# Performance work log

Hardware: AMD Instinct MI355X
Metric: run time of the kernel (lower is better)

The kernel has to match this reference:

```python
import jax, jax.numpy as jnp
import numpy as np

VOCAB = 32000
HID = 128
NUM_LAYERS = 2
B, T = 4, 2048


def setup_inputs() -> dict:
    key = jax.random.key(0)
    ks = jax.random.split(key, 12)
    s = 1.0 / np.sqrt(HID)
    inp = {
        "x": jax.random.randint(ks[0], (B, T), 0, VOCAB, dtype=jnp.int64),
        "hidden": jnp.zeros((NUM_LAYERS, B, HID), jnp.float32),
        "emb": jax.random.normal(ks[1], (VOCAB, HID), jnp.float32),
        "W_ih0": jax.random.uniform(ks[2], (HID, HID), jnp.float32, -s, s),
        "W_hh0": jax.random.uniform(ks[3], (HID, HID), jnp.float32, -s, s),
        "b_ih0": jax.random.uniform(ks[4], (HID,), jnp.float32, -s, s),
        "b_hh0": jax.random.uniform(ks[5], (HID,), jnp.float32, -s, s),
        "W_ih1": jax.random.uniform(ks[6], (HID, HID), jnp.float32, -s, s),
        "W_hh1": jax.random.uniform(ks[7], (HID, HID), jnp.float32, -s, s),
        "b_ih1": jax.random.uniform(ks[8], (HID,), jnp.float32, -s, s),
        "b_hh1": jax.random.uniform(ks[9], (HID,), jnp.float32, -s, s),
        "fc_w": jax.random.uniform(ks[10], (VOCAB, HID), jnp.float32, -s, s),
        "fc_b": jax.random.uniform(ks[11], (VOCAB,), jnp.float32, -s, s),
    }
    return inp


def _rnn_layer(x_seq, h0, W_ih, W_hh, b_ih, b_hh):
    # x_seq: [B, T, H]; h0: [B, H]. Elman RNN with tanh, like nn.RNN.
    def step(h, x_t):
        h_new = jnp.tanh(x_t @ W_ih.T + b_ih + h @ W_hh.T + b_hh)
        return h_new, h_new
    h_last, ys = jax.lax.scan(step, h0, jnp.swapaxes(x_seq, 0, 1))  # scan over T
    return jnp.swapaxes(ys, 0, 1), h_last  # [B,T,H], [B,H]


def reference(x, hidden, emb, W_ih0, W_hh0, b_ih0, b_hh0,
              W_ih1, W_hh1, b_ih1, b_hh1, fc_w, fc_b):
    out = emb[x]  # [B, T, H] embedding lookup
    out, h0 = _rnn_layer(out, hidden[0], W_ih0, W_hh0, b_ih0, b_hh0)
    out, h1 = _rnn_layer(out, hidden[1], W_ih1, W_hh1, b_ih1, b_hh1)
    logits = out @ fc_w.T + fc_b  # [B, T, VOCAB]
    new_hidden = jnp.stack([h0, h1], axis=0)  # [num_layers, B, H]
    return logits, new_hidden
```

## Files before the change

kernel.cpp:

```cpp
#include <hip/hip_runtime.h>

#define BB 4
#define TT 2048
#define HH 128
#define VV 32000

typedef __attribute__((ext_vector_type(8))) _Float16 half8;
typedef __attribute__((ext_vector_type(4))) float floatx4;

__global__ void preact_kernel(const float* __restrict__ src,
                              const int* __restrict__ idx,
                              const float* __restrict__ Wih,
                              const float* __restrict__ b1,
                              const float* __restrict__ b2,
                              float* __restrict__ out) {
    __shared__ float xs[HH];
    int row = blockIdx.x;
    int j = threadIdx.x;
    const float* srow = idx ? (src + (long)idx[row] * HH) : (src + (long)row * HH);
    xs[j] = srow[j];
    __syncthreads();
    const float* wrow = Wih + j * HH;
    float a0 = 0.f, a1 = 0.f, a2 = 0.f, a3 = 0.f;
#pragma unroll
    for (int k = 0; k < HH; k += 4) {
        float4 w = *(const float4*)(wrow + k);
        a0 += w.x * xs[k + 0];
        a1 += w.y * xs[k + 1];
        a2 += w.z * xs[k + 2];
        a3 += w.w * xs[k + 3];
    }
    out[(long)row * HH + j] = (a0 + a1) + (a2 + a3) + b1[j] + b2[j];
}

__global__ void __launch_bounds__(256, 1) rnn_fused_kernel(
        const float* __restrict__ pre0,
        const float* __restrict__ Whh0,
        const float* __restrict__ Wih1,
        const float* __restrict__ Whh1,
        const float* __restrict__ bih1,
        const float* __restrict__ bhh1,
        const float* __restrict__ hin,
        float* __restrict__ out1,
        float* __restrict__ hout) {
    __shared__ float hs0[2][HH];
    __shared__ float hs1[2][HH];
    const int b = blockIdx.x;
    const int tid = threadIdx.x;
    const int l = tid & 63;
    const int half = l >> 5;
    const int j = (tid >> 6) * 32 + (l & 31);

    float w0r[64];
    {
        const float* s = Whh0 + j * HH + half * 64;
#pragma unroll
        for (int q = 0; q < 16; q++) {
            float4 v = *(const float4*)(s + q * 4);
            w0r[4 * q + 0] = v.x; w0r[4 * q + 1] = v.y;
            w0r[4 * q + 2] = v.z; w0r[4 * q + 3] = v.w;
        }
    }
    float w1r[128];
    {
        const float* s = (half ? Whh1 : Wih1) + j * HH;
#pragma unroll
        for (int q = 0; q < 32; q++) {
            float4 v = *(const float4*)(s + q * 4);
            w1r[4 * q + 0] = v.x; w1r[4 * q + 1] = v.y;
            w1r[4 * q + 2] = v.z; w1r[4 * q + 3] = v.w;
        }
    }
    const float bias1 = bih1[j] + bhh1[j];

    if (tid < HH) {
        hs0[1][tid] = hin[b * HH + tid];
        hs1[0][tid] = hin[(BB + b) * HH + tid];
    }
    __syncthreads();

    const float* prow = pre0 + ((long)b * TT) * HH + j;
    float pnext = prow[0];
    for (int i = 0; i <= TT; i++) {
        const int rb = (i & 1) ^ 1;
        const int wb = i & 1;
        float p = pnext;
        if (i + 1 < TT) pnext = prow[(long)(i + 1) * HH];

        float a0 = 0.f, a1 = 0.f, a2 = 0.f, a3 = 0.f;
        if (i < TT) {
#pragma unroll
            for (int q = 0; q < 16; q++) {
                float4 h4 = *(const float4*)(&hs0[rb][half * 64 + q * 4]);
                a0 += h4.x * w0r[4 * q + 0];
                a1 += h4.y * w0r[4 * q + 1];
                a2 += h4.z * w0r[4 * q + 2];
                a3 += h4.w * w0r[4 * q + 3];
            }
        }
        float c0 = 0.f, c1 = 0.f, c2 = 0.f, c3 = 0.f;
        if (i >= 1) {
            const float* hsrc = half ? &hs1[rb][0] : &hs0[rb][0];
#pragma unroll
            for (int q = 0; q < 32; q++) {
                float4 h4 = *(const float4*)(hsrc + q * 4);
                c0 += h4.x * w1r[4 * q + 0];
                c1 += h4.y * w1r[4 * q + 1];
                c2 += h4.z * w1r[4 * q + 2];
                c3 += h4.w * w1r[4 * q + 3];
            }
        }
        float acc0 = (a0 + a1) + (a2 + a3);
        float acc1 = (c0 + c1) + (c2 + c3);
        acc0 += __shfl_xor(acc0, 32);
        acc1 += __shfl_xor(acc1, 32);
        float hnew = tanhf(half ? (acc1 + bias1) : (acc0 + p));
        if (half == 0) {
            if (i < TT) hs0[wb][j] = hnew;
        } else {
            if (i >= 1) {
                hs1[wb][j] = hnew;
                out1[((long)b * TT + (i - 1)) * HH + j] = hnew;
            }
        }
        __syncthreads();
    }
    if (tid < HH) {
        hout[b * HH + tid] = hs0[(TT - 1) & 1][tid];
        hout[(BB + b) * HH + tid] = hs1[TT & 1][tid];
    }
}

#define BM 64
#define BN 128
#define LDK 136

__global__ void __launch_bounds__(256) logits_kernel(
        const float* __restrict__ act,
        const float* __restrict__ fcw,
        const float* __restrict__ fcb,
        float* __restrict__ Cout) {
    __shared__ __align__(16) _Float16 As[BM * LDK];
    __shared__ __align__(16) _Float16 Bs[BN * LDK];
    const int bn = blockIdx.x;
    const int bm = blockIdx.y;
    const int tid = threadIdx.x;

#pragma unroll
    for (int s = 0; s < 8; s++) {
        int f = tid + s * 256;
        int r = f >> 5, c4 = f & 31;
        float4 v = *(const float4*)(act + ((long)(bm * BM + r)) * HH + c4 * 4);
        _Float16* d = &As[r * LDK + c4 * 4];
        d[0] = (_Float16)v.x; d[1] = (_Float16)v.y;
        d[2] = (_Float16)v.z; d[3] = (_Float16)v.w;
    }
#pragma unroll
    for (int s = 0; s < 16; s++) {
        int f = tid + s * 256;
        int r = f >> 5, c4 = f & 31;
        float4 v = *(const float4*)(fcw + ((long)(bn * BN + r)) * HH + c4 * 4);
        _Float16* d = &Bs[r * LDK + c4 * 4];
        d[0] = (_Float16)v.x; d[1] = (_Float16)v.y;
        d[2] = (_Float16)v.z; d[3] = (_Float16)v.w;
    }
    __syncthreads();

    const int wv = tid >> 6;
    const int wm = wv >> 1, wn = wv & 1;
    const int r = tid & 15, q = (tid & 63) >> 4;

    floatx4 acc[2][4];
#pragma unroll
    for (int mt = 0; mt < 2; mt++)
#pragma unroll
        for (int nt = 0; nt < 4; nt++) acc[mt][nt] = (floatx4){0.f, 0.f, 0.f, 0.f};

#pragma unroll
    for (int kk = 0; kk < 4; kk++) {
        half8 af[2], bf[4];
#pragma unroll
        for (int mt = 0; mt < 2; mt++)
            af[mt] = *(const half8*)(&As[(wm * 32 + mt * 16 + r) * LDK + kk * 32 + q * 8]);
#pragma unroll
        for (int nt = 0; nt < 4; nt++)
            bf[nt] = *(const half8*)(&Bs[(wn * 64 + nt * 16 + r) * LDK + kk * 32 + q * 8]);
#pragma unroll
        for (int mt = 0; mt < 2; mt++)
#pragma unroll
            for (int nt = 0; nt < 4; nt++)
                acc[mt][nt] = __builtin_amdgcn_mfma_f32_16x16x32_f16(af[mt], bf[nt], acc[mt][nt], 0, 0, 0);
    }

#pragma unroll
    for (int mt = 0; mt < 2; mt++) {
#pragma unroll
        for (int nt = 0; nt < 4; nt++) {
            int gcol = bn * BN + wn * 64 + nt * 16 + r;
            float bias = fcb[gcol];
#pragma unroll
            for (int r4 = 0; r4 < 4; r4++) {
                int grow = bm * BM + wm * 32 + mt * 16 + q * 4 + r4;
                Cout[(long)grow * VV + gcol] = acc[mt][nt][r4] + bias;
            }
        }
    }
}

extern "C" void kernel_launch(void* const* d_in, const int* in_sizes, int n_in,
                              void* d_out, int out_size, void* d_ws, size_t ws_size,
                              hipStream_t stream) {
    const int*   x      = (const int*)d_in[0];
    const float* hidden = (const float*)d_in[1];
    const float* emb    = (const float*)d_in[2];
    const float* Wih0   = (const float*)d_in[3];
    const float* Whh0   = (const float*)d_in[4];
    const float* bih0   = (const float*)d_in[5];
    const float* bhh0   = (const float*)d_in[6];
    const float* Wih1   = (const float*)d_in[7];
    const float* Whh1   = (const float*)d_in[8];
    const float* bih1   = (const float*)d_in[9];
    const float* bhh1   = (const float*)d_in[10];
    const float* fcw    = (const float*)d_in[11];
    const float* fcb    = (const float*)d_in[12];

    float* logits = (float*)d_out;
    float* hout   = logits + (long)BB * TT * VV;

    float* wsA = (float*)d_ws;
    float* ws1 = wsA + (long)BB * TT * HH;

    preact_kernel<<<BB * TT, HH, 0, stream>>>(emb, x, Wih0, bih0, bhh0, wsA);
    rnn_fused_kernel<<<BB, 256, 0, stream>>>(wsA, Whh0, Wih1, Whh1, bih1, bhh1,
                                             hidden, ws1, hout);
    logits_kernel<<<dim3(VV / BN, (BB * TT) / BM), 256, 0, stream>>>(ws1, fcw, fcb, logits);
}
```

Baseline: 3.717 ms.

## Split RNN layers across separate waves in a 512-thread block

The fused two-layer recurrence now runs with 512 threads. Waves 0-3 compute layer 1 and waves 4-7 compute layer 0, so each thread holds only one layer's weights and does one dot product per step instead of two. The cross-half reduction uses permlane32_swap instead of a shuffle, and __syncthreads is replaced by an explicit lgkmcnt wait plus s_barrier. This shortens each serial step's dependency chain but puts twice as many waves through every per-step barrier.

```diff
diff --git a/kernel.cpp b/kernel.cpp
--- a/kernel.cpp
+++ b/kernel.cpp
@@ -33,7 +33,7 @@
     out[(long)row * HH + j] = (a0 + a1) + (a2 + a3) + b1[j] + b2[j];
 }
 
-__global__ void __launch_bounds__(256, 1) rnn_fused_kernel(
+__global__ void __launch_bounds__(512, 1) rnn_fused_kernel(
         const float* __restrict__ pre0,
         const float* __restrict__ Whh0,
         const float* __restrict__ Wih1,
@@ -47,31 +47,31 @@
     __shared__ float hs1[2][HH];
     const int b = blockIdx.x;
     const int tid = threadIdx.x;
+    const int w = tid >> 6;
     const int l = tid & 63;
-    const int half = l >> 5;
-    const int j = (tid >> 6) * 32 + (l & 31);
-
-    float w0r[64];
-    {
-        const float* s = Whh0 + j * HH + half * 64;
+    const int part = l >> 5;
+    const bool isL1 = (w < 4);
+    const int j = (isL1 ? w : (w - 4)) * 32 + (l & 31);
+
+    float wreg[128];
+    if (isL1) {
+        const float* s = (part ? Whh1 : Wih1) + j * HH;
+#pragma unroll
+        for (int q = 0; q < 32; q++) {
+            float4 v = *(const float4*)(s + 4 * q);
+            wreg[4 * q + 0] = v.x; wreg[4 * q + 1] = v.y;
+            wreg[4 * q + 2] = v.z; wreg[4 * q + 3] = v.w;
+        }
+    } else {
+        const float* s = Whh0 + j * HH + part * 64;
 #pragma unroll
         for (int q = 0; q < 16; q++) {
-            float4 v = *(const float4*)(s + q * 4);
-            w0r[4 * q + 0] = v.x; w0r[4 * q + 1] = v.y;
-            w0r[4 * q + 2] = v.z; w0r[4 * q + 3] = v.w;
-        }
-    }
-    float w1r[128];
-    {
-        const float* s = (half ? Whh1 : Wih1) + j * HH;
-#pragma unroll
-        for (int q = 0; q < 32; q++) {
-            float4 v = *(const float4*)(s + q * 4);
-            w1r[4 * q + 0] = v.x; w1r[4 * q + 1] = v.y;
-            w1r[4 * q + 2] = v.z; w1r[4 * q + 3] = v.w;
-        }
-    }
-    const float bias1 = bih1[j] + bhh1[j];
+            float4 v = *(const float4*)(s + 4 * q);
+            wreg[4 * q + 0] = v.x; wreg[4 * q + 1] = v.y;
+            wreg[4 * q + 2] = v.z; wreg[4 * q + 3] = v.w;
+        }
+    }
+    const float bias1 = isL1 ? (bih1[j] + bhh1[j]) : 0.f;
 
     if (tid < HH) {
         hs0[1][tid] = hin[b * HH + tid];
@@ -79,55 +79,60 @@
     }
     __syncthreads();
 
-    const float* prow = pre0 + ((long)b * TT) * HH + j;
-    float pnext = prow[0];
+    const float* prow = pre0 + (long)b * TT * HH + j;
+    float pnext = isL1 ? 0.f : prow[0];
+
     for (int i = 0; i <= TT; i++) {
         const int rb = (i & 1) ^ 1;
         const int wb = i & 1;
         float p = pnext;
-        if (i + 1 < TT) pnext = prow[(long)(i + 1) * HH];
+        if (!isL1 && (i + 1 < TT)) pnext = prow[(long)(i + 1) * HH];
+        const bool active = isL1 ? (i >= 1) : (i < TT);
 
         float a0 = 0.f, a1 = 0.f, a2 = 0.f, a3 = 0.f;
-        if (i < TT) {
-#pragma unroll
-            for (int q = 0; q < 16; q++) {
-                float4 h4 = *(const float4*)(&hs0[rb][half * 64 + q * 4]);
-                a0 += h4.x * w0r[4 * q + 0];
-                a1 += h4.y * w0r[4 * q + 1];
-                a2 += h4.z * w0r[4 * q + 2];
-                a3 += h4.w * w0r[4 * q + 3];
+        if (active) {
+            if (isL1) {
+                const float* hsrc = part ? &hs1[rb][0] : &hs0[rb][0];
+#pragma unroll
+                for (int q = 0; q < 32; q++) {
+                    float4 h4 = *(const float4*)(hsrc + 4 * q);
+                    a0 += h4.x * wreg[4 * q + 0];
+                    a1 += h4.y * wreg[4 * q + 1];
+                    a2 += h4.z * wreg[4 * q + 2];
+                    a3 += h4.w * wreg[4 * q + 3];
+                }
+            } else {
+                const float* hsrc = &hs0[rb][part * 64];
+#pragma unroll
+                for (int q = 0; q < 16; q++) {
+                    float4 h4 = *(const float4*)(hsrc + 4 * q);
+                    a0 += h4.x * wreg[4 * q + 0];
+                    a1 += h4.y * wreg[4 * q + 1];
+                    a2 += h4.z * wreg[4 * q + 2];
+                    a3 += h4.w * wreg[4 * q + 3];
+                }
             }
         }
-        float c0 = 0.f, c1 = 0.f, c2 = 0.f, c3 = 0.f;
-        if (i >= 1) {
-            const float* hsrc = half ? &hs1[rb][0] : &hs0[rb][0];
-#pragma unroll
-            for (int q = 0; q < 32; q++) {
-                float4 h4 = *(const float4*)(hsrc + q * 4);
-                c0 += h4.x * w1r[4 * q + 0];
-                c1 += h4.y * w1r[4 * q + 1];
-                c2 += h4.z * w1r[4 * q + 2];
-                c3 += h4.w * w1r[4 * q + 3];
-            }
-        }
-        float acc0 = (a0 + a1) + (a2 + a3);
-        float acc1 = (c0 + c1) + (c2 + c3);
-        acc0 += __shfl_xor(acc0, 32);
-        acc1 += __shfl_xor(acc1, 32);
-        float hnew = tanhf(half ? (acc1 + bias1) : (acc0 + p));
-        if (half == 0) {
-            if (i < TT) hs0[wb][j] = hnew;
-        } else {
-            if (i >= 1) {
+        float acc = (a0 + a1) + (a2 + a3);
+        auto sw = __builtin_amdgcn_permlane32_swap(
+            __float_as_uint(acc), __float_as_uint(acc), false, false);
+        float full = __uint_as_float(sw[0]) + __uint_as_float(sw[1]);
+        float hnew = tanhf(full + (isL1 ? bias1 : p));
+        if (active && part == 0) {
+            if (isL1) {
                 hs1[wb][j] = hnew;
                 out1[((long)b * TT + (i - 1)) * HH + j] = hnew;
+            } else {
+                hs0[wb][j] = hnew;
             }
         }
-        __syncthreads();
+        asm volatile("s_waitcnt lgkmcnt(0)" ::: "memory");
+        __builtin_amdgcn_s_barrier();
+        asm volatile("" ::: "memory");
     }
     if (tid < HH) {
-        hout[b * HH + tid] = hs0[(TT - 1) & 1][tid];
-        hout[(BB + b) * HH + tid] = hs1[TT & 1][tid];
+        hout[b * HH + tid] = hs0[1][tid];
+        hout[(BB + b) * HH + tid] = hs1[0][tid];
     }
 }
 
@@ -231,7 +236,7 @@
     float* ws1 = wsA + (long)BB * TT * HH;
 
     preact_kernel<<<BB * TT, HH, 0, stream>>>(emb, x, Wih0, bih0, bhh0, wsA);
-    rnn_fused_kernel<<<BB, 256, 0, stream>>>(wsA, Whh0, Wih1, Whh1, bih1, bhh1,
+    rnn_fused_kernel<<<BB, 512, 0, stream>>>(wsA, Whh0, Wih1, Whh1, bih1, bhh1,
                                              hidden, ws1, hout);
     logits_kernel<<<dim3(VV / BN, (BB * TT) / BM), 256, 0, stream>>>(ws1, fcw, fcb, logits);
 }
```

Measured after the change: 3.056 ms. 17.8% less time.
